# Kernel optimization log

Measured on AMD Instinct MI355X. Metric: run time of the kernel, lower is better.

The kernel has to match this reference:

```python
import jax, jax.numpy as jnp
import numpy as np

EMBED_DIM = 1024
NUM_HEAD = 16
HEAD_DIM = EMBED_DIM // NUM_HEAD
SCALE = HEAD_DIM ** -0.5


def setup_inputs() -> dict:
    key = jax.random.key(0)
    ks = jax.random.split(key, 8)
    B, N, K, D = 2, 2048, 2048, EMBED_DIM
    s = D ** -0.5
    return {
        "x": jax.random.normal(ks[0], (B, N, D), jnp.float32),
        "ctx": jax.random.normal(ks[1], (B, K, D), jnp.float32),
        "Wq": jax.random.normal(ks[2], (D, D), jnp.float32) * s,
        "bq": jnp.zeros((D,), jnp.float32),
        "Wkv": jax.random.normal(ks[3], (D, 2 * D), jnp.float32) * s,
        "bkv": jnp.zeros((2 * D,), jnp.float32),
        "Wproj": jax.random.normal(ks[4], (D, D), jnp.float32) * s,
        "bproj": jnp.zeros((D,), jnp.float32),
    }


def reference(x, ctx, Wq, bq, Wkv, bkv, Wproj, bproj):
    B, N, D = x.shape
    K = ctx.shape[1]
    H, hd = NUM_HEAD, HEAD_DIM
    # Q projection -> [B, H, N, hd]
    q = (x @ Wq + bq).reshape(B, N, H, hd).transpose(0, 2, 1, 3)
    # KV projection -> k, v each [B, H, K, hd]
    kv = (ctx @ Wkv + bkv).reshape(B, K, 2, H, hd).transpose(2, 0, 3, 1, 4)
    k, v = kv[0], kv[1]
    # scaled dot-product attention with materialized scores [B, H, N, K]
    attn = jnp.einsum("bhnd,bhkd->bhnk", q * SCALE, k)
    attn = jax.nn.softmax(attn, axis=-1)
    out = jnp.einsum("bhnk,bhkd->bhnd", attn, v)
    out = out.transpose(0, 2, 1, 3).reshape(B, N, D)
    return out @ Wproj + bproj
```

## Files before the change

kernel.cpp:

```cpp
#include <hip/hip_runtime.h>
#include <hip/hip_bf16.h>

typedef __attribute__((ext_vector_type(8))) short bf16x8;
typedef __attribute__((ext_vector_type(4))) float f32x4;
typedef unsigned short u16;
typedef unsigned int u32;

#define NUM_HEAD 16
#define HEAD_DIM 64
#define SEQ_N 2048
#define SEQ_K 2048
#define EMB 1024
#define MROWS 4096
static constexpr float ATTN_SCALE_LOG2E = 0.125f * 1.44269504f;

#if __has_builtin(__builtin_amdgcn_exp2f)
#define EXP2(x) __builtin_amdgcn_exp2f(x)
#else
#define EXP2(x) __expf(0.69314718056f * (x))
#endif

__device__ __forceinline__ u16 f2bf(float f) {
  __hip_bfloat16 h = __float2bfloat16(f);
  return *reinterpret_cast<u16*>(&h);
}

__device__ __forceinline__ void async16(const u16* g, u16* l) {
  __builtin_amdgcn_global_load_lds(
      (const __attribute__((address_space(1))) unsigned int*)g,
      (__attribute__((address_space(3))) unsigned int*)l, 16, 0, 0);
}

__global__ __launch_bounds__(256) void cvt2(const float* __restrict__ x,
                                            const float* __restrict__ ctx,
                                            u16* __restrict__ xb, u16* __restrict__ cb) {
  const int n4 = MROWS * EMB / 4;
  int gid = blockIdx.x * 256 + threadIdx.x;
  const float4* s; ushort4* d; int i;
  if (gid < n4) { s = (const float4*)x;   d = (ushort4*)xb; i = gid; }
  else          { s = (const float4*)ctx; d = (ushort4*)cb; i = gid - n4; }
  float4 v = s[i];
  ushort4 o;
  o.x = f2bf(v.x); o.y = f2bf(v.y); o.z = f2bf(v.z); o.w = f2bf(v.w);
  d[i] = o;
}

__global__ __launch_bounds__(256) void transpose_cvt4(
    const float* __restrict__ Wq, const float* __restrict__ Wkv,
    const float* __restrict__ Wproj,
    u16* __restrict__ Wqt, u16* __restrict__ Wkvt, u16* __restrict__ Wpt) {
  __shared__ float tile[32][33];
  const int z = blockIdx.z;
  const float* W; u16* Wt; int srcN, colbase;
  if (z == 0)      { W = Wq;    Wt = Wqt;                          srcN = 1024; colbase = 0; }
  else if (z == 1) { W = Wkv;   Wt = Wkvt;                         srcN = 2048; colbase = 0; }
  else if (z == 2) { W = Wkv;   Wt = Wkvt + (size_t)1024 * 1024;   srcN = 2048; colbase = 1024; }
  else             { W = Wproj; Wt = Wpt;                          srcN = 1024; colbase = 0; }
  int n0 = blockIdx.x * 32, k0 = blockIdx.y * 32;
  int tx = threadIdx.x & 31, ty = threadIdx.x >> 5;
  #pragma unroll
  for (int i = ty; i < 32; i += 8)
    tile[i][tx] = W[(size_t)(k0 + i) * srcN + colbase + n0 + tx];
  __syncthreads();
  #pragma unroll
  for (int i = ty; i < 32; i += 8)
    Wt[(size_t)(n0 + i) * 1024 + k0 + tx] = f2bf(tile[tx][i]);
}

__global__ __launch_bounds__(256, 3) void gemm_qkv(
    const u16* __restrict__ xb, const u16* __restrict__ cb,
    const u16* __restrict__ Wqt, const u16* __restrict__ Wkvt,
    const float* __restrict__ bq, const float* __restrict__ bkv,
    u16* __restrict__ Qb, u16* __restrict__ Kb, u16* __restrict__ Vtb)
{
  __shared__ alignas(16) u16 smem[(64 + 256) * 64];
  u16* As = smem;
  u16* Bs = smem + 64 * 64;
  const int tid = threadIdx.x;
  const bool isQ = (blockIdx.y < 4);
  const int n0 = (isQ ? blockIdx.y : blockIdx.y - 4) * 256;
  const int m0 = blockIdx.x * 64;
  const u16* A      = isQ ? xb : cb;
  const u16* Wt     = isQ ? Wqt : Wkvt;
  const float* bias = isQ ? bq : bkv;
  const int wave = tid >> 6, lane = tid & 63;
  const int wm = (wave >> 1) * 32, wn = (wave & 1) * 128;
  const int l15 = lane & 15, quad = lane >> 4;

  f32x4 acc[2][8];
  #pragma unroll
  for (int i = 0; i < 2; i++)
    #pragma unroll
    for (int j = 0; j < 8; j++)
      #pragma unroll
      for (int r = 0; r < 4; r++) acc[i][j][r] = 0.0f;

  const int srow = tid >> 3;
  const int scol = (tid & 7) * 8;
  const u16* ag = A + (size_t)(m0 + srow) * EMB + scol;
  const u16* bg = Wt + (size_t)(n0 + srow) * EMB + scol;
  const int ldsoff = tid * 8;

  for (int kt = 0; kt < EMB; kt += 64) {
    #pragma unroll
    for (int s = 0; s < 2; s++)
      async16(ag + (size_t)(s * 32) * EMB + kt, &As[ldsoff + s * 2048]);
    #pragma unroll
    for (int s = 0; s < 8; s++)
      async16(bg + (size_t)(s * 32) * EMB + kt, &Bs[ldsoff + s * 2048]);
    __syncthreads();
    #pragma unroll
    for (int ks = 0; ks < 2; ks++) {
      bf16x8 af[2], bfr[8];
      #pragma unroll
      for (int i = 0; i < 2; i++)
        af[i]  = *(const bf16x8*)&As[(wm + i * 16 + l15) * 64 + ks * 32 + quad * 8];
      #pragma unroll
      for (int j = 0; j < 8; j++)
        bfr[j] = *(const bf16x8*)&Bs[(wn + j * 16 + l15) * 64 + ks * 32 + quad * 8];
      #pragma unroll
      for (int i = 0; i < 2; i++)
        #pragma unroll
        for (int j = 0; j < 8; j++)
          acc[i][j] = __builtin_amdgcn_mfma_f32_16x16x32_bf16(af[i], bfr[j], acc[i][j], 0, 0, 0);
    }
    __syncthreads();
  }

  if (isQ) {
    #pragma unroll
    for (int i = 0; i < 2; i++) {
      #pragma unroll
      for (int j = 0; j < 8; j++) {
        const int gc = n0 + wn + j * 16 + l15;
        const float bv = bias[gc];
        const int h = gc >> 6, d = gc & 63;
        #pragma unroll
        for (int r = 0; r < 4; r++) {
          const int gm = m0 + wm + i * 16 + quad * 4 + r;
          const int bb = gm >> 11, nn = gm & 2047;
          Qb[((size_t)(bb * NUM_HEAD + h) * SEQ_N + nn) * HEAD_DIM + d] =
              f2bf((acc[i][j][r] + bv) * ATTN_SCALE_LOG2E);
        }
      }
    }
  } else {
    const int s = n0 >> 10;
    if (s == 0) {
      #pragma unroll
      for (int i = 0; i < 2; i++) {
        #pragma unroll
        for (int j = 0; j < 8; j++) {
          const int gc = n0 + wn + j * 16 + l15;
          const float bv = bias[gc];
          const int h = gc >> 6, d = gc & 63;
          #pragma unroll
          for (int r = 0; r < 4; r++) {
            const int gm = m0 + wm + i * 16 + quad * 4 + r;
            const int bb = gm >> 11, kk = gm & 2047;
            Kb[((size_t)(bb * NUM_HEAD + h) * SEQ_K + kk) * HEAD_DIM + d] =
                f2bf(acc[i][j][r] + bv);
          }
        }
      }
    } else {
      u16* wbuf = smem + wave * 1280;
      const int gm0 = m0 + wm;
      const int bb = gm0 >> 11;
      const int kk0 = gm0 & 2047;
      const int hbase = ((n0 + wn) >> 6) & 15;
      #pragma unroll
      for (int hh2 = 0; hh2 < 2; hh2++) {
        #pragma unroll
        for (int p = 0; p < 2; p++) {
          #pragma unroll
          for (int jj = 0; jj < 2; jj++) {
            const int j = hh2 * 4 + p * 2 + jj;
            const int gc = n0 + wn + j * 16 + l15;
            const float bv = bias[gc];
            #pragma unroll
            for (int i = 0; i < 2; i++) {
              ushort4 pk;
              pk.x = f2bf(acc[i][j][0] + bv);
              pk.y = f2bf(acc[i][j][1] + bv);
              pk.z = f2bf(acc[i][j][2] + bv);
              pk.w = f2bf(acc[i][j][3] + bv);
              *(ushort4*)&wbuf[(jj * 16 + l15) * 40 + i * 16 + quad * 4] = pk;
            }
          }
          __syncthreads();
          u32* dstu = (u32*)(Vtb +
              ((size_t)(bb * NUM_HEAD + hbase + hh2) * HEAD_DIM + p * 32) * SEQ_K + kk0);
          #pragma unroll
          for (int it = 0; it < 8; it++) {
            const int dd = it * 4 + quad;
            const int kp = l15 * 2;
            u32 v = *(const u32*)&wbuf[dd * 40 + kp];
            dstu[(size_t)dd * (SEQ_K / 2) + (kp >> 1)] = v;
          }
          __syncthreads();
        }
      }
    }
  }
}

__global__ __launch_bounds__(256) void gemm_proj(
    const u16* __restrict__ A, const u16* __restrict__ Wt,
    const float* __restrict__ bias, float* __restrict__ outF)
{
  __shared__ alignas(16) u16 smem[(64 + 128) * 64];
  u16* As = smem;
  u16* Bs = smem + 64 * 64;
  const int tid = threadIdx.x;
  const int n0 = blockIdx.y * 128, m0 = blockIdx.x * 64;
  const int wave = tid >> 6, lane = tid & 63;
  const int wm = (wave >> 1) * 32, wn = (wave & 1) * 64;
  const int l15 = lane & 15, quad = lane >> 4;

  f32x4 acc[2][4];
  #pragma unroll
  for (int i = 0; i < 2; i++)
    #pragma unroll
    for (int j = 0; j < 4; j++)
      #pragma unroll
      for (int r = 0; r < 4; r++) acc[i][j][r] = 0.0f;

  const int srow = tid >> 3;
  const int scol = (tid & 7) * 8;
  const u16* ag = A + (size_t)(m0 + srow) * EMB + scol;
  const u16* bg = Wt + (size_t)(n0 + srow) * EMB + scol;
  const int ldsoff = tid * 8;

  for (int kt = 0; kt < EMB; kt += 64) {
    async16(ag + kt, &As[ldsoff]);
    async16(ag + (size_t)32 * EMB + kt, &As[ldsoff + 2048]);
    #pragma unroll
    for (int s = 0; s < 4; s++)
      async16(bg + (size_t)(s * 32) * EMB + kt, &Bs[ldsoff + s * 2048]);
    __syncthreads();
    #pragma unroll
    for (int ks = 0; ks < 2; ks++) {
      bf16x8 af[2], bfr[4];
      #pragma unroll
      for (int i = 0; i < 2; i++)
        af[i]  = *(const bf16x8*)&As[(wm + i * 16 + l15) * 64 + ks * 32 + quad * 8];
      #pragma unroll
      for (int j = 0; j < 4; j++)
        bfr[j] = *(const bf16x8*)&Bs[(wn + j * 16 + l15) * 64 + ks * 32 + quad * 8];
      #pragma unroll
      for (int i = 0; i < 2; i++)
        #pragma unroll
        for (int j = 0; j < 4; j++)
          acc[i][j] = __builtin_amdgcn_mfma_f32_16x16x32_bf16(af[i], bfr[j], acc[i][j], 0, 0, 0);
    }
    __syncthreads();
  }

  #pragma unroll
  for (int i = 0; i < 2; i++) {
    #pragma unroll
    for (int j = 0; j < 4; j++) {
      const int gc = n0 + wn + j * 16 + l15;
      const float bv = bias[gc];
      #pragma unroll
      for (int r = 0; r < 4; r++) {
        const int gm = m0 + wm + i * 16 + quad * 4 + r;
        outF[(size_t)gm * EMB + gc] = acc[i][j][r] + bv;
      }
    }
  }
}

__global__ __launch_bounds__(256) void attn_kernel(
    const u16* __restrict__ Qb, const u16* __restrict__ Kb,
    const u16* __restrict__ Vtb, u16* __restrict__ Ob)
{
  __shared__ alignas(16) u16 Ks[64 * 72];
  __shared__ alignas(16) u16 Vs[64 * 72];
  __shared__ alignas(16) u16 Ps[4 * 32 * 72];
  const int tid = threadIdx.x;
  const int bh = blockIdx.x;
  const int m0 = blockIdx.y * 128;
  const int wave = tid >> 6, lane = tid & 63;
  const int l15 = lane & 15, quad = lane >> 4;
  const int rowb = m0 + wave * 32;

  bf16x8 bq[2][2];
  #pragma unroll
  for (int rs = 0; rs < 2; rs++) {
    const u16* qp = Qb + ((size_t)bh * SEQ_N + rowb + rs * 16 + l15) * HEAD_DIM + quad * 8;
    bq[rs][0] = *(const bf16x8*)(qp);
    bq[rs][1] = *(const bf16x8*)(qp + 32);
  }

  f32x4 o[2][4];
  #pragma unroll
  for (int rs = 0; rs < 2; rs++)
    #pragma unroll
    for (int dt = 0; dt < 4; dt++)
      #pragma unroll
      for (int r = 0; r < 4; r++) o[rs][dt][r] = 0.0f;
  float l_part[2] = {0.f, 0.f};
  u16* pbuf = Ps + wave * 32 * 72;

  const int kr = tid >> 3;
  const int ko = (tid & 7) * 8;
  const u16* kg = Kb + ((size_t)bh * SEQ_K + kr) * HEAD_DIM + ko;
  const u16* vg = Vtb + ((size_t)bh * HEAD_DIM + kr) * SEQ_K + ko;

  uint4 kA = *(const uint4*)(kg);
  uint4 kB = *(const uint4*)(kg + (size_t)32 * HEAD_DIM);
  uint4 vA = *(const uint4*)(vg);
  uint4 vB = *(const uint4*)(vg + (size_t)32 * SEQ_K);

  for (int kt = 0; kt < SEQ_K; kt += 64) {
    *(uint4*)&Ks[kr * 72 + ko]        = kA;
    *(uint4*)&Ks[(kr + 32) * 72 + ko] = kB;
    *(uint4*)&Vs[kr * 72 + ko]        = vA;
    *(uint4*)&Vs[(kr + 32) * 72 + ko] = vB;
    __syncthreads();

    if (kt + 64 < SEQ_K) {
      kA = *(const uint4*)(kg + (size_t)(kt + 64) * HEAD_DIM);
      kB = *(const uint4*)(kg + (size_t)(kt + 96) * HEAD_DIM);
      vA = *(const uint4*)(vg + kt + 64);
      vB = *(const uint4*)(vg + (size_t)32 * SEQ_K + kt + 64);
    }

    #pragma unroll
    for (int kt4 = 0; kt4 < 4; kt4++) {
      const bf16x8 a0 = *(const bf16x8*)&Ks[(kt4 * 16 + l15) * 72 + quad * 8];
      const bf16x8 a1 = *(const bf16x8*)&Ks[(kt4 * 16 + l15) * 72 + 32 + quad * 8];
      #pragma unroll
      for (int rs = 0; rs < 2; rs++) {
        f32x4 z = {0.f, 0.f, 0.f, 0.f};
        z = __builtin_amdgcn_mfma_f32_16x16x32_bf16(a0, bq[rs][0], z, 0, 0, 0);
        z = __builtin_amdgcn_mfma_f32_16x16x32_bf16(a1, bq[rs][1], z, 0, 0, 0);
        ushort4 pk;
        float p0 = EXP2(z[0]), p1 = EXP2(z[1]);
        float p2 = EXP2(z[2]), p3 = EXP2(z[3]);
        l_part[rs] += (p0 + p1) + (p2 + p3);
        pk.x = f2bf(p0); pk.y = f2bf(p1); pk.z = f2bf(p2); pk.w = f2bf(p3);
        *(ushort4*)&pbuf[(rs * 16 + l15) * 72 + kt4 * 16 + quad * 4] = pk;
      }
    }

    bf16x8 ap[2][2];
    #pragma unroll
    for (int rs = 0; rs < 2; rs++) {
      ap[rs][0] = *(const bf16x8*)&pbuf[(rs * 16 + l15) * 72 + quad * 8];
      ap[rs][1] = *(const bf16x8*)&pbuf[(rs * 16 + l15) * 72 + 32 + quad * 8];
    }
    #pragma unroll
    for (int dt = 0; dt < 4; dt++) {
      const bf16x8 v0 = *(const bf16x8*)&Vs[(dt * 16 + l15) * 72 + quad * 8];
      const bf16x8 v1 = *(const bf16x8*)&Vs[(dt * 16 + l15) * 72 + 32 + quad * 8];
      #pragma unroll
      for (int rs = 0; rs < 2; rs++) {
        o[rs][dt] = __builtin_amdgcn_mfma_f32_16x16x32_bf16(ap[rs][0], v0, o[rs][dt], 0, 0, 0);
        o[rs][dt] = __builtin_amdgcn_mfma_f32_16x16x32_bf16(ap[rs][1], v1, o[rs][dt], 0, 0, 0);
      }
    }
    __syncthreads();
  }

  float lsum[2];
  #pragma unroll
  for (int rs = 0; rs < 2; rs++) {
    float s = l_part[rs];
    s += __shfl_xor(s, 16, 64);
    s += __shfl_xor(s, 32, 64);
    lsum[rs] = s;
  }

  const int bb = bh >> 4, hh = bh & 15;
  #pragma unroll
  for (int rs = 0; rs < 2; rs++) {
    #pragma unroll
    for (int r = 0; r < 4; r++) {
      const float lv = __shfl(lsum[rs], quad * 4 + r, 64);
      const float inv = 1.0f / lv;
      const int gm = rowb + rs * 16 + quad * 4 + r;
      u16* op = Ob + ((size_t)bb * SEQ_N + gm) * EMB + hh * HEAD_DIM;
      #pragma unroll
      for (int dt = 0; dt < 4; dt++)
        op[dt * 16 + l15] = f2bf(o[rs][dt][r] * inv);
    }
  }
}

extern "C" void kernel_launch(void* const* d_in, const int* in_sizes, int n_in,
                              void* d_out, int out_size, void* d_ws, size_t ws_size,
                              hipStream_t stream)
{
  const float* x     = (const float*)d_in[0];
  const float* ctx   = (const float*)d_in[1];
  const float* Wq    = (const float*)d_in[2];
  const float* bq    = (const float*)d_in[3];
  const float* Wkv   = (const float*)d_in[4];
  const float* bkv   = (const float*)d_in[5];
  const float* Wproj = (const float*)d_in[6];
  const float* bproj = (const float*)d_in[7];
  float* out = (float*)d_out;

  char* ws = (char*)d_ws;
  size_t off = 0;
  auto walloc = [&](size_t bytes) -> void* {
    void* p = ws + off;
    off += (bytes + 255) & ~(size_t)255;
    return p;
  };
  u16* xb   = (u16*)walloc((size_t)MROWS * EMB * 2);
  u16* cb   = (u16*)walloc((size_t)MROWS * EMB * 2);
  u16* Wqt  = (u16*)walloc((size_t)EMB * EMB * 2);
  u16* Wkvt = (u16*)walloc((size_t)2 * EMB * EMB * 2);
  u16* Wpt  = (u16*)walloc((size_t)EMB * EMB * 2);
  u16* Qb   = (u16*)walloc((size_t)MROWS * EMB * 2);
  u16* Kb   = (u16*)walloc((size_t)MROWS * EMB * 2);
  u16* Vtb  = (u16*)walloc((size_t)MROWS * EMB * 2);
  u16* Ob   = (u16*)walloc((size_t)MROWS * EMB * 2);

  cvt2<<<8192, 256, 0, stream>>>(x, ctx, xb, cb);
  transpose_cvt4<<<dim3(32, 32, 4), 256, 0, stream>>>(Wq, Wkv, Wproj, Wqt, Wkvt, Wpt);
  gemm_qkv<<<dim3(64, 12), 256, 0, stream>>>(xb, cb, Wqt, Wkvt, bq, bkv, Qb, Kb, Vtb);
  attn_kernel<<<dim3(32, 16), 256, 0, stream>>>(Qb, Kb, Vtb, Ob);
  gemm_proj<<<dim3(64, 8), 256, 0, stream>>>(Ob, Wpt, bproj, out);
}
```

Baseline: 218.6 us.

## Keep softmax probabilities in registers and double-buffer K/V tiles in attention

Computes the PV product directly from the register-held QK^T output by zero-padding bf16x4 operands into the 16x16x32 MFMA, instead of round-tripping P through LDS. The K/V shared-memory tiles become double-buffered so the next tile's stores overlap the current tile's compute, with one barrier per tile. The output transposes to O^T layout so each lane writes four contiguous bf16 values. Half of every PV MFMA now multiplies zeros, which doubles the PV matrix instruction count.

Result: slower. 259.0 us (+18.5%).

```diff
diff --git a/kernel.cpp b/kernel.cpp
--- a/kernel.cpp
+++ b/kernel.cpp
@@ -2,6 +2,7 @@
 #include <hip/hip_bf16.h>
 
 typedef __attribute__((ext_vector_type(8))) short bf16x8;
+typedef __attribute__((ext_vector_type(4))) short bf16x4;
 typedef __attribute__((ext_vector_type(4))) float f32x4;
 typedef unsigned short u16;
 typedef unsigned int u32;
@@ -23,6 +24,12 @@
 __device__ __forceinline__ u16 f2bf(float f) {
   __hip_bfloat16 h = __float2bfloat16(f);
   return *reinterpret_cast<u16*>(&h);
+}
+
+__device__ __forceinline__ f32x4 pv_mfma(bf16x4 va, bf16x4 pb, f32x4 c) {
+  bf16x8 a8 = {va[0], va[1], va[2], va[3], (short)0, (short)0, (short)0, (short)0};
+  bf16x8 b8 = {pb[0], pb[1], pb[2], pb[3], (short)0, (short)0, (short)0, (short)0};
+  return __builtin_amdgcn_mfma_f32_16x16x32_bf16(a8, b8, c, 0, 0, 0);
 }
 
 __device__ __forceinline__ void async16(const u16* g, u16* l) {
@@ -276,9 +283,7 @@
     const u16* __restrict__ Qb, const u16* __restrict__ Kb,
     const u16* __restrict__ Vtb, u16* __restrict__ Ob)
 {
-  __shared__ alignas(16) u16 Ks[64 * 72];
-  __shared__ alignas(16) u16 Vs[64 * 72];
-  __shared__ alignas(16) u16 Ps[4 * 32 * 72];
+  __shared__ alignas(16) u16 smem[2 * 9216];
   const int tid = threadIdx.x;
   const int bh = blockIdx.x;
   const int m0 = blockIdx.y * 128;
@@ -302,90 +307,92 @@
       #pragma unroll
       for (int r = 0; r < 4; r++) o[rs][dt][r] = 0.0f;
   float l_part[2] = {0.f, 0.f};
-  u16* pbuf = Ps + wave * 32 * 72;
 
   const int kr = tid >> 3;
   const int ko = (tid & 7) * 8;
   const u16* kg = Kb + ((size_t)bh * SEQ_K + kr) * HEAD_DIM + ko;
   const u16* vg = Vtb + ((size_t)bh * HEAD_DIM + kr) * SEQ_K + ko;
 
-  uint4 kA = *(const uint4*)(kg);
-  uint4 kB = *(const uint4*)(kg + (size_t)32 * HEAD_DIM);
-  uint4 vA = *(const uint4*)(vg);
-  uint4 vB = *(const uint4*)(vg + (size_t)32 * SEQ_K);
-
-  for (int kt = 0; kt < SEQ_K; kt += 64) {
-    *(uint4*)&Ks[kr * 72 + ko]        = kA;
-    *(uint4*)&Ks[(kr + 32) * 72 + ko] = kB;
-    *(uint4*)&Vs[kr * 72 + ko]        = vA;
-    *(uint4*)&Vs[(kr + 32) * 72 + ko] = vB;
-    __syncthreads();
-
-    if (kt + 64 < SEQ_K) {
-      kA = *(const uint4*)(kg + (size_t)(kt + 64) * HEAD_DIM);
-      kB = *(const uint4*)(kg + (size_t)(kt + 96) * HEAD_DIM);
-      vA = *(const uint4*)(vg + kt + 64);
-      vB = *(const uint4*)(vg + (size_t)32 * SEQ_K + kt + 64);
-    }
-
+  auto loadT = [&](uint4 (&d)[4], int t) {
+    d[0] = *(const uint4*)(kg + (size_t)(t * 64) * HEAD_DIM);
+    d[1] = *(const uint4*)(kg + (size_t)(t * 64 + 32) * HEAD_DIM);
+    d[2] = *(const uint4*)(vg + t * 64);
+    d[3] = *(const uint4*)(vg + (size_t)32 * SEQ_K + t * 64);
+  };
+  auto stage = [&](int buf, const uint4 (&d)[4]) {
+    u16* K = smem + buf * 9216;
+    *(uint4*)&K[kr * 72 + ko]        = d[0];
+    *(uint4*)&K[(kr + 32) * 72 + ko] = d[1];
+    u16* V = K + 4608;
+    *(uint4*)&V[kr * 72 + ko]        = d[2];
+    *(uint4*)&V[(kr + 32) * 72 + ko] = d[3];
+  };
+  auto compute = [&](int buf) {
+    const u16* K = smem + buf * 9216;
+    const u16* V = K + 4608;
     #pragma unroll
     for (int kt4 = 0; kt4 < 4; kt4++) {
-      const bf16x8 a0 = *(const bf16x8*)&Ks[(kt4 * 16 + l15) * 72 + quad * 8];
-      const bf16x8 a1 = *(const bf16x8*)&Ks[(kt4 * 16 + l15) * 72 + 32 + quad * 8];
+      const bf16x8 a0 = *(const bf16x8*)&K[(kt4 * 16 + l15) * 72 + quad * 8];
+      const bf16x8 a1 = *(const bf16x8*)&K[(kt4 * 16 + l15) * 72 + 32 + quad * 8];
+      bf16x4 pf[2];
       #pragma unroll
       for (int rs = 0; rs < 2; rs++) {
         f32x4 z = {0.f, 0.f, 0.f, 0.f};
         z = __builtin_amdgcn_mfma_f32_16x16x32_bf16(a0, bq[rs][0], z, 0, 0, 0);
         z = __builtin_amdgcn_mfma_f32_16x16x32_bf16(a1, bq[rs][1], z, 0, 0, 0);
-        ushort4 pk;
         float p0 = EXP2(z[0]), p1 = EXP2(z[1]);
         float p2 = EXP2(z[2]), p3 = EXP2(z[3]);
         l_part[rs] += (p0 + p1) + (p2 + p3);
-        pk.x = f2bf(p0); pk.y = f2bf(p1); pk.z = f2bf(p2); pk.w = f2bf(p3);
-        *(ushort4*)&pbuf[(rs * 16 + l15) * 72 + kt4 * 16 + quad * 4] = pk;
-      }
-    }
-
-    bf16x8 ap[2][2];
-    #pragma unroll
-    for (int rs = 0; rs < 2; rs++) {
-      ap[rs][0] = *(const bf16x8*)&pbuf[(rs * 16 + l15) * 72 + quad * 8];
-      ap[rs][1] = *(const bf16x8*)&pbuf[(rs * 16 + l15) * 72 + 32 + quad * 8];
-    }
-    #pragma unroll
-    for (int dt = 0; dt < 4; dt++) {
-      const bf16x8 v0 = *(const bf16x8*)&Vs[(dt * 16 + l15) * 72 + quad * 8];
-      const bf16x8 v1 = *(const bf16x8*)&Vs[(dt * 16 + l15) * 72 + 32 + quad * 8];
-      #pragma unroll
-      for (int rs = 0; rs < 2; rs++) {
-        o[rs][dt] = __builtin_amdgcn_mfma_f32_16x16x32_bf16(ap[rs][0], v0, o[rs][dt], 0, 0, 0);
-        o[rs][dt] = __builtin_amdgcn_mfma_f32_16x16x32_bf16(ap[rs][1], v1, o[rs][dt], 0, 0, 0);
-      }
-    }
-    __syncthreads();
-  }
-
-  float lsum[2];
+        bf16x4 pk;
+        pk[0] = (short)f2bf(p0); pk[1] = (short)f2bf(p1);
+        pk[2] = (short)f2bf(p2); pk[3] = (short)f2bf(p3);
+        pf[rs] = pk;
+      }
+      #pragma unroll
+      for (int dt = 0; dt < 4; dt++) {
+        const bf16x4 va = *(const bf16x4*)&V[(dt * 16 + l15) * 72 + kt4 * 16 + quad * 4];
+        o[0][dt] = pv_mfma(va, pf[0], o[0][dt]);
+        o[1][dt] = pv_mfma(va, pf[1], o[1][dt]);
+      }
+    }
+  };
+
+  uint4 ra[4], rb[4];
+  loadT(ra, 0);
+  stage(0, ra);
+  loadT(rb, 1);
+  __syncthreads();
+
+  for (int t = 0; t < 32; t += 2) {
+    stage(1, rb);
+    if (t + 2 < 32) loadT(ra, t + 2);
+    compute(0);
+    __syncthreads();
+    if (t + 2 < 32) {
+      stage(0, ra);
+      if (t + 3 < 32) loadT(rb, t + 3);
+    }
+    compute(1);
+    __syncthreads();
+  }
+
+  const int bb = bh >> 4, hh = bh & 15;
   #pragma unroll
   for (int rs = 0; rs < 2; rs++) {
     float s = l_part[rs];
     s += __shfl_xor(s, 16, 64);
     s += __shfl_xor(s, 32, 64);
-    lsum[rs] = s;
-  }
-
-  const int bb = bh >> 4, hh = bh & 15;
-  #pragma unroll
-  for (int rs = 0; rs < 2; rs++) {
-    #pragma unroll
-    for (int r = 0; r < 4; r++) {
-      const float lv = __shfl(lsum[rs], quad * 4 + r, 64);
-      const float inv = 1.0f / lv;
-      const int gm = rowb + rs * 16 + quad * 4 + r;
-      u16* op = Ob + ((size_t)bb * SEQ_N + gm) * EMB + hh * HEAD_DIM;
-      #pragma unroll
-      for (int dt = 0; dt < 4; dt++)
-        op[dt * 16 + l15] = f2bf(o[rs][dt][r] * inv);
+    const float inv = 1.0f / s;
+    const int gm = rowb + rs * 16 + l15;
+    u16* op = Ob + ((size_t)bb * SEQ_N + gm) * EMB + hh * HEAD_DIM;
+    #pragma unroll
+    for (int dt = 0; dt < 4; dt++) {
+      ushort4 pk;
+      pk.x = f2bf(o[rs][dt][0] * inv);
+      pk.y = f2bf(o[rs][dt][1] * inv);
+      pk.z = f2bf(o[rs][dt][2] * inv);
+      pk.w = f2bf(o[rs][dt][3] * inv);
+      *(ushort4*)&op[dt * 16 + quad * 4] = pk;
     }
   }
 }
```
